# Optimization experiments

Hardware: AMD Instinct MI355X
Metric: run time of the kernel (lower is better)

## Reference

```python
import jax, jax.numpy as jnp
import numpy as np
import math

B_TOPK = 8  # self.B
NEG = -1e9  # numerically-equivalent stand-in for float('-inf') mask


def setup_inputs() -> dict:
    key = jax.random.key(0)
    ks = jax.random.split(key, 12)
    b, s, d, d_low = 4, 2048, 128, 16
    sc = 1.0 / math.sqrt(d)
    return {
        "queries": jax.random.normal(ks[0], (b, s, d), jnp.float32),
        "keys": jax.random.normal(ks[1], (b, s, d), jnp.float32),
        "values": jax.random.normal(ks[2], (b, s, d), jnp.float32),
        "valid_lens": jax.random.randint(ks[3], (b, s), 0, s, jnp.int32),
        "Wq_low": jax.random.normal(ks[4], (d, d_low), jnp.float32) * sc,
        "bq_low": jnp.zeros((d_low,), jnp.float32),
        "Wk_low": jax.random.normal(ks[5], (d, d_low), jnp.float32) * sc,
        "bk_low": jnp.zeros((d_low,), jnp.float32),
        "Wq_high": jax.random.normal(ks[6], (d, d_low), jnp.float32) * sc,
        "bq_high": jnp.zeros((d_low,), jnp.float32),
        "Wk_high": jax.random.normal(ks[7], (d, d_low), jnp.float32) * sc,
        "bk_high": jnp.zeros((d_low,), jnp.float32),
    }


def reference(queries, keys, values, valid_lens, Wq_low, bq_low, Wk_low, bk_low,
              Wq_high, bq_high, Wk_high, bk_high):
    b, s, d = queries.shape
    d_low = Wq_low.shape[1]
    scale = 1.0 / math.sqrt(d_low)

    # low-rank scores [b, sq, sk]
    q_low = queries @ Wq_low + bq_low
    k_low = keys @ Wk_low + bk_low
    scores_low = jnp.einsum('bqe,bke->bqk', q_low, k_low) * scale

    # mask: scatter -inf at (batch, valid_lens[b,k], k) along dim 1 (as in torch code)
    vl = jnp.clip(valid_lens, 0, s - 1)                      # [b, sk]
    mask = vl[:, None, :] == jnp.arange(s)[None, :, None]    # [b, sq, sk]
    scores_masked = jnp.where(mask, scores_low + NEG, scores_low)

    # top-B keys per query row (over key axis)
    _, topk_idx = jax.lax.top_k(scores_masked, B_TOPK)       # [b, s, B]

    # gather top-B queries/keys per row, project to d_low, rank-d_low correction score
    bi = jnp.arange(b)[:, None, None]
    q_high = queries[bi, topk_idx]                           # [b, s, B, d]
    k_high = keys[bi, topk_idx]                              # [b, s, B, d]
    q_proj = q_high @ Wq_high + bq_high                      # [b, s, B, d_low]
    k_proj = k_high @ Wk_high + bk_high
    score_high = jnp.sum(q_proj * k_proj, axis=-1) * scale   # [b, s, B]

    # scatter corrected scores back into the masked score matrix (dim 2)
    si = jnp.arange(s)[None, :, None]
    corrected = scores_masked.at[bi, si, topk_idx].set(score_high)

    # masked_softmax with valid_lens applies softmax over dim=1
    attn = jax.nn.softmax(corrected, axis=1)
    return jnp.einsum('bqk,bkd->bqd', attn, values)
```

## Files before the change

kernel.cpp:

```cpp
#include <hip/hip_runtime.h>
#include <float.h>
#include <math.h>

#define SEQ 2048
#define NB 4
#define DIM 128
#define DL 16
#define NEGV (-1e9f)
#define TOPK 8

#define QT 128
#define KC 64
#define QCH 64

typedef unsigned long long u64;
typedef __attribute__((ext_vector_type(8))) short short8;
typedef __attribute__((ext_vector_type(4))) float f32x4;

__device__ __forceinline__ void top8_insert(float* s, float key) {
    #pragma unroll
    for (int i = 0; i < 8; ++i) {
        float a = s[i];
        s[i] = fmaxf(a, key);
        key  = fminf(a, key);
    }
}

__device__ __forceinline__ float top8_merge(float* s) {
    #pragma unroll
    for (int off = 1; off < 64; off <<= 1) {
        float o[8], t[8];
        #pragma unroll
        for (int i = 0; i < 8; ++i)
            o[i] = __shfl_xor(s[i], off, 64);
        #pragma unroll
        for (int i = 0; i < 8; ++i)
            t[i] = fmaxf(s[i], o[7 - i]);
        #pragma unroll
        for (int i = 0; i < 4; ++i) {
            float a = t[i], c = t[i + 4];
            t[i] = fmaxf(a, c); t[i + 4] = fminf(a, c);
        }
        #pragma unroll
        for (int g2 = 0; g2 < 8; g2 += 4) {
            float a = t[g2], c = t[g2 + 2];
            t[g2] = fmaxf(a, c); t[g2 + 2] = fminf(a, c);
            a = t[g2 + 1]; c = t[g2 + 3];
            t[g2 + 1] = fmaxf(a, c); t[g2 + 3] = fminf(a, c);
        }
        #pragma unroll
        for (int g1 = 0; g1 < 8; g1 += 2) {
            float a = t[g1], c = t[g1 + 1];
            t[g1] = fmaxf(a, c); t[g1 + 1] = fminf(a, c);
        }
        #pragma unroll
        for (int i = 0; i < 8; ++i) s[i] = t[i];
    }
    return s[7];
}

__device__ __forceinline__ unsigned bf16_rne(float x) {
    unsigned u = __float_as_uint(x);
    return (u + 0x7FFFu + ((u >> 16) & 1u)) >> 16;
}

__global__ __launch_bounds__(256) void proj_kernel(
    const float* __restrict__ q, const float* __restrict__ k,
    const float* __restrict__ Wql, const float* __restrict__ bql,
    const float* __restrict__ Wkl, const float* __restrict__ bkl,
    const float* __restrict__ Wqh, const float* __restrict__ bqh,
    const float* __restrict__ Wkh, const float* __restrict__ bkh,
    float* __restrict__ q_low, float* __restrict__ k_low,
    float* __restrict__ sh)
{
    __shared__ float Ws[4][DIM * DL];
    __shared__ float rowq[16][DIM];
    __shared__ float rowk[16][DIM];
    int tid = threadIdx.x;
    for (int i = tid; i < DIM * DL; i += 256) {
        Ws[0][i] = Wql[i];
        Ws[1][i] = Wkl[i];
        Ws[2][i] = Wqh[i];
        Ws[3][i] = Wkh[i];
    }
    int r0 = blockIdx.x * 16;
    for (int i = tid; i < 16 * DIM; i += 256) {
        int rr = i >> 7, cc = i & 127;
        rowq[rr][cc] = q[(size_t)(r0 + rr) * DIM + cc];
        rowk[rr][cc] = k[(size_t)(r0 + rr) * DIM + cc];
    }
    __syncthreads();
    int g = tid >> 4;
    int e = tid & 15;
    float aql = 0.f, akl = 0.f, aqh = 0.f, akh = 0.f;
    #pragma unroll 8
    for (int i = 0; i < DIM; ++i) {
        float qv = rowq[g][i], kv = rowk[g][i];
        aql = fmaf(qv, Ws[0][i * DL + e], aql);
        akl = fmaf(kv, Ws[1][i * DL + e], akl);
        aqh = fmaf(qv, Ws[2][i * DL + e], aqh);
        akh = fmaf(kv, Ws[3][i * DL + e], akh);
    }
    int t = r0 + g;
    q_low[(size_t)t * DL + e] = aql + bql[e];
    k_low[(size_t)t * DL + e] = akl + bkl[e];
    float qp = aqh + bqh[e];
    float kp = akh + bkh[e];
    float prod = qp * kp;
    #pragma unroll
    for (int off = 8; off >= 1; off >>= 1)
        prod += __shfl_xor(prod, off, 16);
    if (e == 0) sh[t] = 0.25f * prod;
}

__global__ __launch_bounds__(256) void vsplit_kernel(
    const float* __restrict__ V, unsigned short* __restrict__ VH,
    unsigned short* __restrict__ VL)
{
    __shared__ float T[32][33];
    int kb = blockIdx.x * 32, db = blockIdx.y * 32, b = blockIdx.z;
    int tid = threadIdx.x;
    {
        int r = tid >> 3, cg = tid & 7;
        float4 v = *(const float4*)(V + ((size_t)b * SEQ + kb + r) * DIM + db + cg * 4);
        T[r][cg * 4 + 0] = v.x; T[r][cg * 4 + 1] = v.y;
        T[r][cg * 4 + 2] = v.z; T[r][cg * 4 + 3] = v.w;
    }
    __syncthreads();
    int dr = tid >> 3, kg = tid & 7;
    unsigned h[4], l[4];
    #pragma unroll
    for (int j = 0; j < 4; ++j) {
        float f = T[kg * 4 + j][dr];
        unsigned hi = bf16_rne(f);
        float hf = __uint_as_float(hi << 16);
        unsigned lo = bf16_rne(f - hf);
        h[j] = hi; l[j] = lo;
    }
    size_t o = ((size_t)b * DIM + db + dr) * SEQ + kb + kg * 4;
    *(uint2*)(VH + o) = make_uint2(h[0] | (h[1] << 16), h[2] | (h[3] << 16));
    *(uint2*)(VL + o) = make_uint2(l[0] | (l[1] << 16), l[2] | (l[3] << 16));
}

__global__ __launch_bounds__(256) void score_topk10(
    const float* __restrict__ q_low, const float* __restrict__ k_low,
    const int* __restrict__ valid_lens,
    float* __restrict__ Smat, float* __restrict__ thrv)
{
    __shared__ float KT[2][256 * DL];

    int tid  = threadIdx.x;
    int lane = tid & 63;
    int wv   = tid >> 6;
    int row0 = __builtin_amdgcn_readfirstlane(blockIdx.x * 8 + wv * 2);
    int b    = row0 >> 11;
    int qi0  = row0 & (SEQ - 1);
    int qi1  = qi0 + 1;

    float qv0[16], qv1[16];
    {
        const float* qp0 = q_low + (size_t)row0 * DL;
        #pragma unroll
        for (int e = 0; e < 16; ++e) { qv0[e] = qp0[e]; qv1[e] = qp0[DL + e]; }
    }

    const float4* kb4 = (const float4*)(k_low + (size_t)b * SEQ * DL);
    const int*    vlb = valid_lens + (size_t)b * SEQ;
    float* Srow0 = Smat + (size_t)row0 * SEQ;
    float* Srow1 = Srow0 + SEQ;

    float s0[8], s1[8];
    #pragma unroll
    for (int i = 0; i < 8; ++i) { s0[i] = -FLT_MAX; s1[i] = -FLT_MAX; }

    float4 stg[4];
    #pragma unroll
    for (int i = 0; i < 4; ++i) stg[i] = kb4[tid + i * 256];
    {
        float4* d = (float4*)KT[0];
        #pragma unroll
        for (int i = 0; i < 4; ++i) d[tid + i * 256] = stg[i];
    }
    __syncthreads();

    for (int c = 0; c < 8; ++c) {
        if (c < 7) {
            #pragma unroll
            for (int i = 0; i < 4; ++i)
                stg[i] = kb4[(c + 1) * 1024 + tid + i * 256];
        }
        int vli[4];
        #pragma unroll
        for (int j = 0; j < 4; ++j)
            vli[j] = vlb[c * 256 + lane + j * 64];

        const float* Kc = KT[c & 1];
        #pragma unroll
        for (int j = 0; j < 4; ++j) {
            int ccol = lane + j * 64;
            int col  = c * 256 + ccol;
            const float4* kp4 = (const float4*)(Kc + ccol * DL);
            float4 v0 = kp4[0], v1 = kp4[1], v2 = kp4[2], v3 = kp4[3];

            float a0 = 0.f, a1 = 0.f;
            a0 = fmaf(qv0[0],  v0.x, a0); a1 = fmaf(qv1[0],  v0.x, a1);
            a0 = fmaf(qv0[1],  v0.y, a0); a1 = fmaf(qv1[1],  v0.y, a1);
            a0 = fmaf(qv0[2],  v0.z, a0); a1 = fmaf(qv1[2],  v0.z, a1);
            a0 = fmaf(qv0[3],  v0.w, a0); a1 = fmaf(qv1[3],  v0.w, a1);
            a0 = fmaf(qv0[4],  v1.x, a0); a1 = fmaf(qv1[4],  v1.x, a1);
            a0 = fmaf(qv0[5],  v1.y, a0); a1 = fmaf(qv1[5],  v1.y, a1);
            a0 = fmaf(qv0[6],  v1.z, a0); a1 = fmaf(qv1[6],  v1.z, a1);
            a0 = fmaf(qv0[7],  v1.w, a0); a1 = fmaf(qv1[7],  v1.w, a1);
            a0 = fmaf(qv0[8],  v2.x, a0); a1 = fmaf(qv1[8],  v2.x, a1);
            a0 = fmaf(qv0[9],  v2.y, a0); a1 = fmaf(qv1[9],  v2.y, a1);
            a0 = fmaf(qv0[10], v2.z, a0); a1 = fmaf(qv1[10], v2.z, a1);
            a0 = fmaf(qv0[11], v2.w, a0); a1 = fmaf(qv1[11], v2.w, a1);
            a0 = fmaf(qv0[12], v3.x, a0); a1 = fmaf(qv1[12], v3.x, a1);
            a0 = fmaf(qv0[13], v3.y, a0); a1 = fmaf(qv1[13], v3.y, a1);
            a0 = fmaf(qv0[14], v3.z, a0); a1 = fmaf(qv1[14], v3.z, a1);
            a0 = fmaf(qv0[15], v3.w, a0); a1 = fmaf(qv1[15], v3.w, a1);
            a0 *= 0.25f; a1 *= 0.25f;

            int v = vli[j];
            v = v < 0 ? 0 : (v > SEQ - 1 ? SEQ - 1 : v);
            if (v == qi0) a0 += NEGV;
            if (v == qi1) a1 += NEGV;
            Srow0[col] = a0;
            Srow1[col] = a1;
            top8_insert(s0, a0);
            top8_insert(s1, a1);
        }
        if (c < 7) {
            float* d0 = KT[(c + 1) & 1];
            float4* d = (float4*)d0;
            #pragma unroll
            for (int i = 0; i < 4; ++i) d[tid + i * 256] = stg[i];
            __syncthreads();
        }
    }

    float t80 = top8_merge(s0);
    float t81 = top8_merge(s1);
    if (lane == 0) {
        thrv[row0]     = t80;
        thrv[row0 + 1] = t81;
    }
}

__global__ __launch_bounds__(256) void colred_partial(
    const float* __restrict__ Smat, const float* __restrict__ thrv,
    const float* __restrict__ sh,
    float* __restrict__ pm, float* __restrict__ pl)
{
    int kcol = blockIdx.x * 256 + threadIdx.x;
    int qc = blockIdx.y;
    int b  = blockIdx.z;
    const float* Sp  = Smat + (size_t)b * SEQ * SEQ + (size_t)(qc * QCH) * SEQ + kcol;
    const float* thb = thrv + (size_t)b * SEQ + qc * QCH;
    float shk = sh[(size_t)b * SEQ + kcol];
    float m = -FLT_MAX, l = 0.f;
    #pragma unroll 4
    for (int qq = 0; qq < QCH; ++qq) {
        float v = Sp[(size_t)qq * SEQ];
        float t = thb[qq];
        v = (v >= t) ? shk : v;
        float nm = fmaxf(m, v);
        l = l * __expf(m - nm) + __expf(v - nm);
        m = nm;
    }
    pm[((size_t)b * 32 + qc) * SEQ + kcol] = m;
    pl[((size_t)b * 32 + qc) * SEQ + kcol] = l;
}

__global__ __launch_bounds__(256) void colred_final(
    const float* __restrict__ pm, const float* __restrict__ pl,
    float* __restrict__ cmax, float* __restrict__ cinv)
{
    int idx = blockIdx.x * 256 + threadIdx.x;
    int b = idx >> 11, kcol = idx & (SEQ - 1);
    float m = -FLT_MAX, l = 0.f;
    #pragma unroll
    for (int c = 0; c < 32; ++c) {
        float mm = pm[((size_t)b * 32 + c) * SEQ + kcol];
        float ll = pl[((size_t)b * 32 + c) * SEQ + kcol];
        float nm = fmaxf(m, mm);
        l = l * __expf(m - nm) + ll * __expf(mm - nm);
        m = nm;
    }
    cmax[idx] = m;
    cinv[idx] = 1.f / l;
}

__global__ __launch_bounds__(256) void out_mfma(
    const float* __restrict__ Smat, const unsigned short* __restrict__ VH,
    const unsigned short* __restrict__ VL,
    const float* __restrict__ cmax, const float* __restrict__ cinv,
    const float* __restrict__ thrv, const float* __restrict__ sh,
    float* __restrict__ dst, int krange)
{
    __shared__ unsigned int VtH[DIM * 32];
    __shared__ unsigned int VtL[DIM * 32];

    int tid  = threadIdx.x;
    int w    = tid >> 6;
    int lane = tid & 63;
    int ln   = lane & 15;
    int quad = lane >> 4;
    int q0   = blockIdx.x * QT;
    int ksid = blockIdx.y;
    int b    = blockIdx.z;
    int kbeg = ksid * krange;

    const float* Sb = Smat + (size_t)b * SEQ * SEQ;
    const unsigned short* VHb = VH + (size_t)b * DIM * SEQ;
    const unsigned short* VLb = VL + (size_t)b * DIM * SEQ;
    const float* cm  = cmax + (size_t)b * SEQ;
    const float* ci  = cinv + (size_t)b * SEQ;
    const float* shb = sh + (size_t)b * SEQ;

    float thrm[2];
    #pragma unroll
    for (int mt = 0; mt < 2; ++mt)
        thrm[mt] = thrv[(size_t)b * SEQ + q0 + w * 32 + mt * 16 + ln];

    f32x4 acc[2][8];
    #pragma unroll
    for (int mt = 0; mt < 2; ++mt)
        #pragma unroll
        for (int nt = 0; nt < 8; ++nt)
            acc[mt][nt] = (f32x4){0.f, 0.f, 0.f, 0.f};

    int sd0   = tid >> 3;
    int skseg = tid & 7;

    for (int k0 = kbeg; k0 < kbeg + krange; k0 += KC) {
        #pragma unroll
        for (int it = 0; it < 4; ++it) {
            int d = sd0 + it * 32;
            size_t go = (size_t)d * SEQ + k0 + skseg * 8;
            uint4 hv = *(const uint4*)(VHb + go);
            uint4 lv = *(const uint4*)(VLb + go);
            int wa = d * 32 + ((skseg ^ (d & 7)) << 2);
            *(uint4*)&VtH[wa] = hv;
            *(uint4*)&VtL[wa] = lv;
        }

        short8 Ah[2][2], Al[2][2];
        #pragma unroll
        for (int ks = 0; ks < 2; ++ks) {
            int kk = k0 + ks * 32 + quad * 8;
            float4 cma = *(const float4*)(cm + kk);
            float4 cmb = *(const float4*)(cm + kk + 4);
            float4 cia = *(const float4*)(ci + kk);
            float4 cib = *(const float4*)(ci + kk + 4);
            float4 sha = *(const float4*)(shb + kk);
            float4 shx = *(const float4*)(shb + kk + 4);
            #pragma unroll
            for (int mt = 0; mt < 2; ++mt) {
                const float* Sp = Sb + (size_t)(q0 + w * 32 + mt * 16 + ln) * SEQ + kk;
                float4 sa = *(const float4*)Sp;
                float4 sb = *(const float4*)(Sp + 4);
                float t = thrm[mt];
                float e0 = (sa.x >= t) ? sha.x : sa.x;
                float e1 = (sa.y >= t) ? sha.y : sa.y;
                float e2 = (sa.z >= t) ? sha.z : sa.z;
                float e3 = (sa.w >= t) ? sha.w : sa.w;
                float e4 = (sb.x >= t) ? shx.x : sb.x;
                float e5 = (sb.y >= t) ? shx.y : sb.y;
                float e6 = (sb.z >= t) ? shx.z : sb.z;
                float e7 = (sb.w >= t) ? shx.w : sb.w;
                float p[8];
                p[0] = __expf(e0 - cma.x) * cia.x;
                p[1] = __expf(e1 - cma.y) * cia.y;
                p[2] = __expf(e2 - cma.z) * cia.z;
                p[3] = __expf(e3 - cma.w) * cia.w;
                p[4] = __expf(e4 - cmb.x) * cib.x;
                p[5] = __expf(e5 - cmb.y) * cib.y;
                p[6] = __expf(e6 - cmb.z) * cib.z;
                p[7] = __expf(e7 - cmb.w) * cib.w;
                #pragma unroll
                for (int j = 0; j < 8; ++j) {
                    unsigned hi = bf16_rne(p[j]);
                    float hf = __uint_as_float(hi << 16);
                    unsigned lo = bf16_rne(p[j] - hf);
                    Ah[mt][ks][j] = (short)hi;
                    Al[mt][ks][j] = (short)lo;
                }
            }
        }
        __syncthreads();

        #pragma unroll
        for (int nt = 0; nt < 8; ++nt) {
            int d = nt * 16 + ln;
            #pragma unroll
            for (int ks = 0; ks < 2; ++ks) {
                int kseg = ks * 4 + quad;
                int wa = d * 32 + ((kseg ^ (d & 7)) << 2);
                short8 bh = *(short8*)&VtH[wa];
                short8 bl = *(short8*)&VtL[wa];
                #pragma unroll
                for (int mt = 0; mt < 2; ++mt) {
                    acc[mt][nt] = __builtin_amdgcn_mfma_f32_16x16x32_bf16(
                        Ah[mt][ks], bh, acc[mt][nt], 0, 0, 0);
                    acc[mt][nt] = __builtin_amdgcn_mfma_f32_16x16x32_bf16(
                        Al[mt][ks], bh, acc[mt][nt], 0, 0, 0);
                    acc[mt][nt] = __builtin_amdgcn_mfma_f32_16x16x32_bf16(
                        Ah[mt][ks], bl, acc[mt][nt], 0, 0, 0);
                }
            }
        }
        __syncthreads();
    }

    float* dp = dst + (size_t)ksid * ((size_t)NB * SEQ * DIM)
                    + (size_t)b * SEQ * DIM;
    #pragma unroll
    for (int mt = 0; mt < 2; ++mt) {
        #pragma unroll
        for (int r = 0; r < 4; ++r) {
            float* o = dp + (size_t)(q0 + w * 32 + mt * 16 + quad * 4 + r) * DIM + ln;
            #pragma unroll
            for (int nt = 0; nt < 8; ++nt)
                o[nt * 16] = acc[mt][nt][r];
        }
    }
}

__global__ __launch_bounds__(256) void reduce_kernel(
    const float* __restrict__ part, float* __restrict__ out, int ksplit)
{
    int idx = blockIdx.x * 256 + threadIdx.x;
    const float4* p = (const float4*)part;
    float4 a = p[idx];
    for (int s = 1; s < ksplit; ++s) {
        float4 q = p[(size_t)idx + (size_t)s * 262144];
        a.x += q.x; a.y += q.y; a.z += q.z; a.w += q.w;
    }
    ((float4*)out)[idx] = a;
}

extern "C" void kernel_launch(void* const* d_in, const int* in_sizes, int n_in,
                              void* d_out, int out_size, void* d_ws, size_t ws_size,
                              hipStream_t stream)
{
    const float* queries = (const float*)d_in[0];
    const float* keys    = (const float*)d_in[1];
    const float* values  = (const float*)d_in[2];
    const int*   valid   = (const int*)d_in[3];
    const float* Wql = (const float*)d_in[4];
    const float* bql = (const float*)d_in[5];
    const float* Wkl = (const float*)d_in[6];
    const float* bkl = (const float*)d_in[7];
    const float* Wqh = (const float*)d_in[8];
    const float* bqh = (const float*)d_in[9];
    const float* Wkh = (const float*)d_in[10];
    const float* bkh = (const float*)d_in[11];

    char* ws = (char*)d_ws;
    float* Smat  = (float*)(ws);
    float* q_low = (float*)(ws + 67108864);
    float* k_low = (float*)(ws + 67633152);
    float* sh    = (float*)(ws + 68157440);
    float* thrv  = (float*)(ws + 68190208);
    float* cmax  = (float*)(ws + 68222976);
    float* cinv  = (float*)(ws + 68255744);
    unsigned short* VthH = (unsigned short*)(ws + 68288512);
    unsigned short* VthL = (unsigned short*)(ws + 70385664);
    const size_t part_off = 72482816;
    float* pm    = (float*)(ws + part_off);
    float* pl    = (float*)(ws + part_off + 1048576);
    float* part  = (float*)(ws + part_off);

    const size_t part_sz  = (size_t)NB * SEQ * DIM * 4;
    int ksplit = 1;
    if      (ws_size >= part_off + 8 * part_sz) ksplit = 8;
    else if (ws_size >= part_off + 4 * part_sz) ksplit = 4;
    else if (ws_size >= part_off + 2 * part_sz) ksplit = 2;

    proj_kernel<<<dim3((NB * SEQ) / 16), 256, 0, stream>>>(
        queries, keys, Wql, bql, Wkl, bkl, Wqh, bqh, Wkh, bkh, q_low, k_low, sh);

    vsplit_kernel<<<dim3(SEQ / 32, DIM / 32, NB), 256, 0, stream>>>(
        values, VthH, VthL);

    score_topk10<<<dim3((NB * SEQ) / 8), 256, 0, stream>>>(
        q_low, k_low, valid, Smat, thrv);

    colred_partial<<<dim3(SEQ / 256, 32, NB), 256, 0, stream>>>(
        Smat, thrv, sh, pm, pl);

    colred_final<<<dim3((NB * SEQ) / 256), 256, 0, stream>>>(pm, pl, cmax, cinv);

    if (ksplit == 1) {
        out_mfma<<<dim3(SEQ / QT, 1, NB), 256, 0, stream>>>(
            Smat, VthH, VthL, cmax, cinv, thrv, sh, (float*)d_out, SEQ);
    } else {
        out_mfma<<<dim3(SEQ / QT, ksplit, NB), 256, 0, stream>>>(
            Smat, VthH, VthL, cmax, cinv, thrv, sh, part, SEQ / ksplit);
        reduce_kernel<<<(NB * SEQ * DIM / 4) / 256, 256, 0, stream>>>(
            part, (float*)d_out, ksplit);
    }
}
```

Before: 167.7 us.

## Compute low-rank scores with split-bf16 MFMA instead of scalar FMA

The projection kernel now splits q_low and k_low into three-term bf16 hi/mid/lo pieces, packed into K=32 operand layouts. The score kernel computes each 16x16 score tile with three bf16 MFMA instructions, which approximates fp32 accuracy, in place of scalar FMA loops over LDS-staged keys. Each block handles 16 query rows with four waves splitting the key columns, and per-row top-8 is merged across lanes and waves through shared memory. This cuts ALU work on the score computation. In exchange the Smat stores become strided 16-column writes, the score precision is slightly lower, and there is an extra cross-wave reduction step.

```diff
diff --git a/kernel.cpp b/kernel.cpp
--- a/kernel.cpp
+++ b/kernel.cpp
@@ -26,9 +26,9 @@
     }
 }
 
-__device__ __forceinline__ float top8_merge(float* s) {
-    #pragma unroll
-    for (int off = 1; off < 64; off <<= 1) {
+__device__ __forceinline__ float top8_merge16(float* s) {
+    #pragma unroll
+    for (int off = 1; off < 16; off <<= 1) {
         float o[8], t[8];
         #pragma unroll
         for (int i = 0; i < 8; ++i)
@@ -70,7 +70,9 @@
     const float* __restrict__ Wkl, const float* __restrict__ bkl,
     const float* __restrict__ Wqh, const float* __restrict__ bqh,
     const float* __restrict__ Wkh, const float* __restrict__ bkh,
-    float* __restrict__ q_low, float* __restrict__ k_low,
+    unsigned short* __restrict__ qA1, unsigned short* __restrict__ qA2,
+    unsigned short* __restrict__ qA3,
+    unsigned short* __restrict__ kB1, unsigned short* __restrict__ kB2,
     float* __restrict__ sh)
 {
     __shared__ float Ws[4][DIM * DL];
@@ -102,8 +104,30 @@
         akh = fmaf(kv, Ws[3][i * DL + e], akh);
     }
     int t = r0 + g;
-    q_low[(size_t)t * DL + e] = aql + bql[e];
-    k_low[(size_t)t * DL + e] = akl + bkl[e];
+    float qv = aql + bql[e];
+    float kv = akl + bkl[e];
+
+    unsigned q1 = bf16_rne(qv);
+    float q1f = __uint_as_float(q1 << 16);
+    float qr1 = qv - q1f;
+    unsigned q2 = bf16_rne(qr1);
+    float q2f = __uint_as_float(q2 << 16);
+    unsigned q3 = bf16_rne(qr1 - q2f);
+
+    unsigned k1 = bf16_rne(kv);
+    float k1f = __uint_as_float(k1 << 16);
+    float kr1 = kv - k1f;
+    unsigned k2 = bf16_rne(kr1);
+    float k2f = __uint_as_float(k2 << 16);
+    unsigned k3 = bf16_rne(kr1 - k2f);
+
+    size_t pb = (size_t)t * 32;
+    qA1[pb + e] = (unsigned short)q1; qA1[pb + 16 + e] = (unsigned short)q2;
+    qA2[pb + e] = (unsigned short)q2; qA2[pb + 16 + e] = (unsigned short)q1;
+    qA3[pb + e] = (unsigned short)q1; qA3[pb + 16 + e] = (unsigned short)q3;
+    kB1[pb + e] = (unsigned short)k1; kB1[pb + 16 + e] = (unsigned short)k2;
+    kB2[pb + e] = (unsigned short)k3; kB2[pb + 16 + e] = (unsigned short)k1;
+
     float qp = aqh + bqh[e];
     float kp = akh + bkh[e];
     float prod = qp * kp;
@@ -142,108 +166,88 @@
     *(uint2*)(VL + o) = make_uint2(l[0] | (l[1] << 16), l[2] | (l[3] << 16));
 }
 
-__global__ __launch_bounds__(256) void score_topk10(
-    const float* __restrict__ q_low, const float* __restrict__ k_low,
+__global__ __launch_bounds__(256) void score_mfma(
+    const unsigned short* __restrict__ qA1, const unsigned short* __restrict__ qA2,
+    const unsigned short* __restrict__ qA3,
+    const unsigned short* __restrict__ kB1, const unsigned short* __restrict__ kB2,
     const int* __restrict__ valid_lens,
     float* __restrict__ Smat, float* __restrict__ thrv)
 {
-    __shared__ float KT[2][256 * DL];
+    __shared__ float red[4][16][8];
 
     int tid  = threadIdx.x;
     int lane = tid & 63;
     int wv   = tid >> 6;
-    int row0 = __builtin_amdgcn_readfirstlane(blockIdx.x * 8 + wv * 2);
+    int c15  = lane & 15;
+    int g    = lane >> 4;
+    int row0 = __builtin_amdgcn_readfirstlane(blockIdx.x * 16);
     int b    = row0 >> 11;
     int qi0  = row0 & (SEQ - 1);
-    int qi1  = qi0 + 1;
-
-    float qv0[16], qv1[16];
-    {
-        const float* qp0 = q_low + (size_t)row0 * DL;
-        #pragma unroll
-        for (int e = 0; e < 16; ++e) { qv0[e] = qp0[e]; qv1[e] = qp0[DL + e]; }
-    }
-
-    const float4* kb4 = (const float4*)(k_low + (size_t)b * SEQ * DL);
-    const int*    vlb = valid_lens + (size_t)b * SEQ;
-    float* Srow0 = Smat + (size_t)row0 * SEQ;
-    float* Srow1 = Srow0 + SEQ;
-
-    float s0[8], s1[8];
-    #pragma unroll
-    for (int i = 0; i < 8; ++i) { s0[i] = -FLT_MAX; s1[i] = -FLT_MAX; }
-
-    float4 stg[4];
-    #pragma unroll
-    for (int i = 0; i < 4; ++i) stg[i] = kb4[tid + i * 256];
-    {
-        float4* d = (float4*)KT[0];
-        #pragma unroll
-        for (int i = 0; i < 4; ++i) d[tid + i * 256] = stg[i];
+
+    size_t aoff = (size_t)(row0 + c15) * 32 + g * 8;
+    short8 A1 = *(const short8*)(qA1 + aoff);
+    short8 A2 = *(const short8*)(qA2 + aoff);
+    short8 A3 = *(const short8*)(qA3 + aoff);
+
+    const unsigned short* kb1 = kB1 + (size_t)b * SEQ * 32;
+    const unsigned short* kb2 = kB2 + (size_t)b * SEQ * 32;
+    const int* vlb = valid_lens + (size_t)b * SEQ;
+
+    float s8[4][8];
+    #pragma unroll
+    for (int r = 0; r < 4; ++r)
+        #pragma unroll
+        for (int i = 0; i < 8; ++i) s8[r][i] = -FLT_MAX;
+
+    int rowg[4];
+    #pragma unroll
+    for (int r = 0; r < 4; ++r) rowg[r] = qi0 + g * 4 + r;
+
+    for (int ct = wv * 32; ct < wv * 32 + 32; ++ct) {
+        int col = ct * 16 + c15;
+        size_t boff = (size_t)col * 32 + g * 8;
+        short8 B1 = *(const short8*)(kb1 + boff);
+        short8 B2 = *(const short8*)(kb2 + boff);
+
+        f32x4 acc = (f32x4){0.f, 0.f, 0.f, 0.f};
+        acc = __builtin_amdgcn_mfma_f32_16x16x32_bf16(A1, B1, acc, 0, 0, 0);
+        acc = __builtin_amdgcn_mfma_f32_16x16x32_bf16(A2, B1, acc, 0, 0, 0);
+        acc = __builtin_amdgcn_mfma_f32_16x16x32_bf16(A3, B2, acc, 0, 0, 0);
+
+        int vl = vlb[col];
+        vl = vl < 0 ? 0 : (vl > SEQ - 1 ? SEQ - 1 : vl);
+
+        float* So = Smat + (size_t)(row0 + g * 4) * SEQ + col;
+        #pragma unroll
+        for (int r = 0; r < 4; ++r) {
+            float v = 0.25f * acc[r];
+            if (vl == rowg[r]) v += NEGV;
+            So[(size_t)r * SEQ] = v;
+            top8_insert(s8[r], v);
+        }
+    }
+
+    #pragma unroll
+    for (int r = 0; r < 4; ++r) top8_merge16(s8[r]);
+
+    if (c15 == 0) {
+        #pragma unroll
+        for (int r = 0; r < 4; ++r)
+            #pragma unroll
+            for (int i = 0; i < 8; ++i)
+                red[wv][g * 4 + r][i] = s8[r][i];
     }
     __syncthreads();
-
-    for (int c = 0; c < 8; ++c) {
-        if (c < 7) {
+    if (tid < 16) {
+        float fin[8];
+        #pragma unroll
+        for (int i = 0; i < 8; ++i) fin[i] = red[0][tid][i];
+        #pragma unroll
+        for (int w2 = 1; w2 < 4; ++w2)
             #pragma unroll
-            for (int i = 0; i < 4; ++i)
-                stg[i] = kb4[(c + 1) * 1024 + tid + i * 256];
-        }
-        int vli[4];
-        #pragma unroll
-        for (int j = 0; j < 4; ++j)
-            vli[j] = vlb[c * 256 + lane + j * 64];
-
-        const float* Kc = KT[c & 1];
-        #pragma unroll
-        for (int j = 0; j < 4; ++j) {
-            int ccol = lane + j * 64;
-            int col  = c * 256 + ccol;
-            const float4* kp4 = (const float4*)(Kc + ccol * DL);
-            float4 v0 = kp4[0], v1 = kp4[1], v2 = kp4[2], v3 = kp4[3];
-
-            float a0 = 0.f, a1 = 0.f;
-            a0 = fmaf(qv0[0],  v0.x, a0); a1 = fmaf(qv1[0],  v0.x, a1);
-            a0 = fmaf(qv0[1],  v0.y, a0); a1 = fmaf(qv1[1],  v0.y, a1);
-            a0 = fmaf(qv0[2],  v0.z, a0); a1 = fmaf(qv1[2],  v0.z, a1);
-            a0 = fmaf(qv0[3],  v0.w, a0); a1 = fmaf(qv1[3],  v0.w, a1);
-            a0 = fmaf(qv0[4],  v1.x, a0); a1 = fmaf(qv1[4],  v1.x, a1);
-            a0 = fmaf(qv0[5],  v1.y, a0); a1 = fmaf(qv1[5],  v1.y, a1);
-            a0 = fmaf(qv0[6],  v1.z, a0); a1 = fmaf(qv1[6],  v1.z, a1);
-            a0 = fmaf(qv0[7],  v1.w, a0); a1 = fmaf(qv1[7],  v1.w, a1);
-            a0 = fmaf(qv0[8],  v2.x, a0); a1 = fmaf(qv1[8],  v2.x, a1);
-            a0 = fmaf(qv0[9],  v2.y, a0); a1 = fmaf(qv1[9],  v2.y, a1);
-            a0 = fmaf(qv0[10], v2.z, a0); a1 = fmaf(qv1[10], v2.z, a1);
-            a0 = fmaf(qv0[11], v2.w, a0); a1 = fmaf(qv1[11], v2.w, a1);
-            a0 = fmaf(qv0[12], v3.x, a0); a1 = fmaf(qv1[12], v3.x, a1);
-            a0 = fmaf(qv0[13], v3.y, a0); a1 = fmaf(qv1[13], v3.y, a1);
-            a0 = fmaf(qv0[14], v3.z, a0); a1 = fmaf(qv1[14], v3.z, a1);
-            a0 = fmaf(qv0[15], v3.w, a0); a1 = fmaf(qv1[15], v3.w, a1);
-            a0 *= 0.25f; a1 *= 0.25f;
-
-            int v = vli[j];
-            v = v < 0 ? 0 : (v > SEQ - 1 ? SEQ - 1 : v);
-            if (v == qi0) a0 += NEGV;
-            if (v == qi1) a1 += NEGV;
-            Srow0[col] = a0;
-            Srow1[col] = a1;
-            top8_insert(s0, a0);
-            top8_insert(s1, a1);
-        }
-        if (c < 7) {
-            float* d0 = KT[(c + 1) & 1];
-            float4* d = (float4*)d0;
-            #pragma unroll
-            for (int i = 0; i < 4; ++i) d[tid + i * 256] = stg[i];
-            __syncthreads();
-        }
-    }
-
-    float t80 = top8_merge(s0);
-    float t81 = top8_merge(s1);
-    if (lane == 0) {
-        thrv[row0]     = t80;
-        thrv[row0 + 1] = t81;
+            for (int i = 0; i < 8; ++i)
+                top8_insert(fin, red[w2][tid][i]);
+        thrv[row0 + tid] = fin[7];
     }
 }
 
@@ -458,16 +462,19 @@
     const float* bkh = (const float*)d_in[11];
 
     char* ws = (char*)d_ws;
-    float* Smat  = (float*)(ws);
-    float* q_low = (float*)(ws + 67108864);
-    float* k_low = (float*)(ws + 67633152);
-    float* sh    = (float*)(ws + 68157440);
-    float* thrv  = (float*)(ws + 68190208);
-    float* cmax  = (float*)(ws + 68222976);
-    float* cinv  = (float*)(ws + 68255744);
-    unsigned short* VthH = (unsigned short*)(ws + 68288512);
-    unsigned short* VthL = (unsigned short*)(ws + 70385664);
-    const size_t part_off = 72482816;
+    float* Smat = (float*)(ws);
+    unsigned short* qA1 = (unsigned short*)(ws + 67108864);
+    unsigned short* qA2 = (unsigned short*)(ws + 67633152);
+    unsigned short* qA3 = (unsigned short*)(ws + 68157440);
+    unsigned short* kB1 = (unsigned short*)(ws + 68681728);
+    unsigned short* kB2 = (unsigned short*)(ws + 69206016);
+    float* sh    = (float*)(ws + 69730304);
+    float* thrv  = (float*)(ws + 69763072);
+    float* cmax  = (float*)(ws + 69795840);
+    float* cinv  = (float*)(ws + 69828608);
+    unsigned short* VthH = (unsigned short*)(ws + 69861376);
+    unsigned short* VthL = (unsigned short*)(ws + 71958528);
+    const size_t part_off = 74055680;
     float* pm    = (float*)(ws + part_off);
     float* pl    = (float*)(ws + part_off + 1048576);
     float* part  = (float*)(ws + part_off);
@@ -479,13 +486,14 @@
     else if (ws_size >= part_off + 2 * part_sz) ksplit = 2;
 
     proj_kernel<<<dim3((NB * SEQ) / 16), 256, 0, stream>>>(
-        queries, keys, Wql, bql, Wkl, bkl, Wqh, bqh, Wkh, bkh, q_low, k_low, sh);
+        queries, keys, Wql, bql, Wkl, bkl, Wqh, bqh, Wkh, bkh,
+        qA1, qA2, qA3, kB1, kB2, sh);
 
     vsplit_kernel<<<dim3(SEQ / 32, DIM / 32, NB), 256, 0, stream>>>(
         values, VthH, VthL);
 
-    score_topk10<<<dim3((NB * SEQ) / 8), 256, 0, stream>>>(
-        q_low, k_low, valid, Smat, thrv);
+    score_mfma<<<dim3((NB * SEQ) / 16), 256, 0, stream>>>(
+        qA1, qA2, qA3, kB1, kB2, valid, Smat, thrv);
 
     colred_partial<<<dim3(SEQ / 256, 32, NB), 256, 0, stream>>>(
         Smat, thrv, sh, pm, pl);
```

Result: faster. 163.5 us (-2.5%).
